# Performance work log

Hardware: AMD Instinct MI355X
Metric: run time of the kernel (lower is better)

Reference implementation:

```python
import jax, jax.numpy as jnp
import numpy as np

HID = 64        # HIDDEN_DIM
SLOTS = 6       # MEMORY_SLOTS
V = 64          # VOCAB_SIZE
NH = 2          # attention heads
THRESH = 0.5    # STAGE1_THRESH
EPS = 1e-5      # LayerNorm eps (torch default)


def setup_inputs() -> dict:
    key = jax.random.key(0)
    ks = jax.random.split(key, 16)
    B, L = 64, 1024
    def n(k, shape, s=0.05):
        return jax.random.normal(k, shape, jnp.float32) * s
    return {
        'seq':    jax.random.randint(ks[0], (B, L), 0, V),
        'query':  jax.random.randint(ks[1], (B,), 0, V),
        'target': jax.random.randint(ks[2], (B,), 0, V),
        # TinyEncoder params
        'embed':   n(ks[3], (V, HID)),
        'wqkv':    n(ks[4], (3 * HID, HID)), 'bqkv': jnp.zeros(3 * HID, jnp.float32),
        'wo_attn': n(ks[5], (HID, HID)),     'bo_attn': jnp.zeros(HID, jnp.float32),
        'w_ff1':   n(ks[6], (2 * HID, HID)), 'b_ff1': jnp.zeros(2 * HID, jnp.float32),
        'w_ff2':   n(ks[7], (HID, 2 * HID)), 'b_ff2': jnp.zeros(HID, jnp.float32),
        'g1': jnp.ones(HID, jnp.float32), 'be1': jnp.zeros(HID, jnp.float32),
        'g2': jnp.ones(HID, jnp.float32), 'be2': jnp.zeros(HID, jnp.float32),
        # gates
        'w_s1': n(ks[8], (1, HID)), 'b_s1': jnp.zeros(1, jnp.float32),
        'w_s2': n(ks[9], (1, HID)), 'b_s2': jnp.zeros(1, jnp.float32),
        # MemoryReader
        'w_qr': n(ks[10], (HID, HID)), 'b_qr': jnp.zeros(HID, jnp.float32),
        'w_or': n(ks[11], (V, HID)),   'b_or': jnp.zeros(V, jnp.float32),
        # query embedding
        'q_embed': n(ks[12], (V, HID)),
    }


def _layernorm(x, g, b):
    m = x.mean(-1, keepdims=True)
    v = ((x - m) ** 2).mean(-1, keepdims=True)
    return (x - m) * jax.lax.rsqrt(v + EPS) * g + b


def _mha(h, wqkv, bqkv, wo, bo):
    B, L, H = h.shape
    d = H // NH
    qkv = h @ wqkv.T + bqkv                      # [B,L,3H]
    q, k, v = jnp.split(qkv, 3, axis=-1)
    q = q.reshape(B, L, NH, d)
    k = k.reshape(B, L, NH, d)
    v = v.reshape(B, L, NH, d)
    scores = jnp.einsum('bqhd,bkhd->bhqk', q, k) / jnp.sqrt(jnp.float32(d))
    w = jax.nn.softmax(scores, axis=-1)          # [B,NH,L,L]
    o = jnp.einsum('bhqk,bkhd->bqhd', w, v).reshape(B, L, H)
    return o @ wo.T + bo


def reference(seq, query, target, embed, wqkv, bqkv, wo_attn, bo_attn,
              w_ff1, b_ff1, w_ff2, b_ff2, g1, be1, g2, be2,
              w_s1, b_s1, w_s2, b_s2, w_qr, b_qr, w_or, b_or, q_embed):
    # --- TinyEncoder ---
    h = embed[seq]                                           # [B,L,H]
    a = _mha(h, wqkv, bqkv, wo_attn, bo_attn)
    h = _layernorm(h + a, g1, be1)
    ff = jax.nn.relu(h @ w_ff1.T + b_ff1) @ w_ff2.T + b_ff2
    hidden = _layernorm(h + ff, g2, be2)                     # [B,L,H]

    # --- two-stage selection (vectorized; dead s1-branch elided) ---
    s1 = jax.nn.sigmoid(jnp.squeeze(hidden @ w_s1.T + b_s1, -1))   # [B,L]
    keep = (s1 > THRESH).astype(hidden.dtype)
    s2 = jax.nn.sigmoid(jnp.squeeze(hidden @ w_s2.T + b_s2, -1))
    s2f = s2 * keep
    _, topk = jax.lax.top_k(s2f, SLOTS)                            # [B,SLOTS]

    # --- gather memory slots ---
    mem = jnp.take_along_axis(hidden, topk[:, :, None], axis=1)    # [B,SLOTS,H]

    # --- MemoryReader ---
    q_h = q_embed[query]                                           # [B,H]
    q = q_h @ w_qr.T + b_qr                                        # [B,H]
    scores = (q[:, None, :] * mem).sum(-1) / jnp.sqrt(jnp.float32(HID))  # [B,SLOTS]
    w = jax.nn.softmax(scores, axis=-1)
    ctx = (w[:, :, None] * mem).sum(1)                             # [B,H]
    logits = ctx @ w_or.T + b_or                                   # [B,V]

    # --- cross entropy (mean) ---
    logp = jax.nn.log_softmax(logits, axis=-1)
    loss = -jnp.take_along_axis(logp, target[:, None], axis=1).mean()
    return loss
```

## Files before the change

kernel.cpp:

```cpp
#include <hip/hip_runtime.h>

#define DEV __device__ __forceinline__

DEV float wsum(float v){
  #pragma unroll
  for (int o = 32; o; o >>= 1) v += __shfl_xor(v, o, 64);
  return v;
}
DEV float wmax(float v){
  #pragma unroll
  for (int o = 32; o; o >>= 1) v = fmaxf(v, __shfl_xor(v, o, 64));
  return v;
}

__global__ __launch_bounds__(1024) void k_prep(
    const int* __restrict__ seq, const float* __restrict__ embed,
    const float* __restrict__ wqkv, const float* __restrict__ bqkv,
    float* __restrict__ qkv_tab, float* __restrict__ cnt_f,
    float* __restrict__ out){
  const int b = blockIdx.x, tid = threadIdx.x;
  if (b == 0 && tid == 0) out[0] = 0.f;
  __shared__ float emb[64];
  __shared__ int hh[64];
  if (tid < 64){ emb[tid] = embed[b*64 + tid]; hh[tid] = 0; }
  __syncthreads();
  atomicAdd(&hh[seq[b*1024 + tid]], 1);
  if (tid < 192){
    const float4* w4 = (const float4*)(wqkv + tid*64);
    float a0 = bqkv[tid], a1 = 0.f, a2 = 0.f, a3 = 0.f;
    #pragma unroll
    for (int k = 0; k < 16; k += 4){
      float4 wa = w4[k],   wb = w4[k+1], wc = w4[k+2], wd = w4[k+3];
      a0 += wa.x*emb[4*k]    + wa.y*emb[4*k+1]  + wa.z*emb[4*k+2]  + wa.w*emb[4*k+3];
      a1 += wb.x*emb[4*k+4]  + wb.y*emb[4*k+5]  + wb.z*emb[4*k+6]  + wb.w*emb[4*k+7];
      a2 += wc.x*emb[4*k+8]  + wc.y*emb[4*k+9]  + wc.z*emb[4*k+10] + wc.w*emb[4*k+11];
      a3 += wd.x*emb[4*k+12] + wd.y*emb[4*k+13] + wd.z*emb[4*k+14] + wd.w*emb[4*k+15];
    }
    qkv_tab[b*192 + tid] = (a0+a1)+(a2+a3);
  }
  __syncthreads();
  if (tid < 64) cnt_f[b*64 + tid] = (float)hh[tid];
}

__global__ __launch_bounds__(1024, 4) void k_enc(
    const float* __restrict__ qkv_tab, const float* __restrict__ cnt_f,
    const float* __restrict__ embed,
    const float* __restrict__ wo_attn, const float* __restrict__ bo_attn,
    const float* __restrict__ w_ff1, const float* __restrict__ b_ff1,
    const float* __restrict__ w_ff2, const float* __restrict__ b_ff2,
    const float* __restrict__ g1, const float* __restrict__ be1,
    const float* __restrict__ g2, const float* __restrict__ be2,
    const float* __restrict__ w_s1, const float* __restrict__ b_s1,
    const float* __restrict__ w_s2, const float* __restrict__ b_s2,
    float* __restrict__ hidden_tab, float* __restrict__ s2f_tab){
  const int b = blockIdx.x >> 2, quarter = blockIdx.x & 3;
  const int tid = threadIdx.x, wave = tid >> 6, lane = tid & 63;

  __shared__ float k_lds[64*65];
  __shared__ float v_lds[64*65];
  __shared__ float wo_lds[64*65];
  __shared__ float ff1_lds[128*65];
  __shared__ float ff2_lds[64*129];
  __shared__ float cnt_lds[64];
  __shared__ float xbuf[16][64];
  __shared__ float pbuf[16][128];

  for (int i = tid; i < 4096; i += 1024){
    int r = i >> 6, c = i & 63;
    k_lds[r*65 + c]  = qkv_tab[r*192 + 64 + c];
    v_lds[r*65 + c]  = qkv_tab[r*192 + 128 + c];
    wo_lds[r*65 + c] = wo_attn[i];
  }
  for (int i = tid; i < 8192; i += 1024){
    ff1_lds[(i >> 6)*65 + (i & 63)]   = w_ff1[i];
    ff2_lds[(i >> 7)*129 + (i & 127)] = w_ff2[i];
  }
  if (tid < 64) cnt_lds[tid] = cnt_f[b*64 + tid];
  __syncthreads();

  const float g1v = g1[lane],  be1v = be1[lane];
  const float g2v = g2[lane],  be2v = be2[lane];
  const float bov = bo_attn[lane], bf2v = b_ff2[lane];
  const float bf1a = b_ff1[lane], bf1b = b_ff1[64 + lane];
  const float ws1v = w_s1[lane], ws2v = w_s2[lane];
  const float bs1 = b_s1[0], bs2 = b_s2[0];
  const float cme = cnt_lds[lane];
  const bool  pres = cme > 0.f;
  const float sc = 0.17677669529663687f;
  const int   tok = quarter*16 + wave;

  const float qreg = qkv_tab[tok*192 + lane];
  xbuf[wave][lane] = qreg;
  __builtin_amdgcn_wave_barrier();
  float s0a = 0.f, s0b = 0.f, s1a = 0.f, s1b = 0.f;
  #pragma unroll
  for (int d = 0; d < 32; d += 2){
    s0a += xbuf[wave][d]      * k_lds[lane*65 + d];
    s0b += xbuf[wave][d+1]    * k_lds[lane*65 + d + 1];
    s1a += xbuf[wave][32+d]   * k_lds[lane*65 + 32 + d];
    s1b += xbuf[wave][32+d+1] * k_lds[lane*65 + 32 + d + 1];
  }
  float s0  = (s0a + s0b) * sc;
  float s1v = (s1a + s1b) * sc;
  float m0 = wmax(pres ? s0  : -1e30f);
  float m1 = wmax(pres ? s1v : -1e30f);
  float p0 = pres ? cme * __expf(s0  - m0) : 0.f;
  float p1 = pres ? cme * __expf(s1v - m1) : 0.f;
  float d0 = wsum(p0), d1 = wsum(p1);
  pbuf[wave][lane] = p0; pbuf[wave][64 + lane] = p1;
  __builtin_amdgcn_wave_barrier();
  const int pb = (lane & 32) << 1;
  float o0 = 0.f, o1 = 0.f, o2 = 0.f, o3 = 0.f;
  #pragma unroll
  for (int t = 0; t < 64; t += 4){
    o0 += pbuf[wave][pb + t]     * v_lds[t*65 + lane];
    o1 += pbuf[wave][pb + t + 1] * v_lds[(t+1)*65 + lane];
    o2 += pbuf[wave][pb + t + 2] * v_lds[(t+2)*65 + lane];
    o3 += pbuf[wave][pb + t + 3] * v_lds[(t+3)*65 + lane];
  }
  float o = ((o0 + o1) + (o2 + o3)) / (lane < 32 ? d0 : d1);
  xbuf[wave][lane] = o;
  __builtin_amdgcn_wave_barrier();
  float a0 = bov, a1 = 0.f, a2 = 0.f, a3 = 0.f;
  #pragma unroll
  for (int k = 0; k < 64; k += 4){
    a0 += wo_lds[lane*65 + k]     * xbuf[wave][k];
    a1 += wo_lds[lane*65 + k + 1] * xbuf[wave][k+1];
    a2 += wo_lds[lane*65 + k + 2] * xbuf[wave][k+2];
    a3 += wo_lds[lane*65 + k + 3] * xbuf[wave][k+3];
  }
  float a = (a0 + a1) + (a2 + a3);
  float x = embed[tok*64 + lane] + a;
  float mu = wsum(x) * 0.015625f;
  float xm = x - mu;
  float var = wsum(xm*xm) * 0.015625f;
  float xn = xm * rsqrtf(var + 1e-5f) * g1v + be1v;
  xbuf[wave][lane] = xn;
  __builtin_amdgcn_wave_barrier();
  float y0a = bf1a, y0b = 0.f, y1a = bf1b, y1b = 0.f;
  #pragma unroll
  for (int k = 0; k < 64; k += 2){
    float xk0 = xbuf[wave][k], xk1 = xbuf[wave][k+1];
    y0a += ff1_lds[lane*65 + k]          * xk0;
    y0b += ff1_lds[lane*65 + k + 1]      * xk1;
    y1a += ff1_lds[(lane+64)*65 + k]     * xk0;
    y1b += ff1_lds[(lane+64)*65 + k + 1] * xk1;
  }
  float y0 = fmaxf(y0a + y0b, 0.f), y1 = fmaxf(y1a + y1b, 0.f);
  pbuf[wave][lane] = y0; pbuf[wave][64 + lane] = y1;
  __builtin_amdgcn_wave_barrier();
  float z0 = bf2v, z1 = 0.f, z2 = 0.f, z3 = 0.f;
  #pragma unroll
  for (int j = 0; j < 128; j += 4){
    z0 += ff2_lds[lane*129 + j]     * pbuf[wave][j];
    z1 += ff2_lds[lane*129 + j + 1] * pbuf[wave][j+1];
    z2 += ff2_lds[lane*129 + j + 2] * pbuf[wave][j+2];
    z3 += ff2_lds[lane*129 + j + 3] * pbuf[wave][j+3];
  }
  float z = (z0 + z1) + (z2 + z3);
  float r = xn + z;
  float mu2 = wsum(r) * 0.015625f;
  float rm = r - mu2;
  float var2 = wsum(rm*rm) * 0.015625f;
  float hid = rm * rsqrtf(var2 + 1e-5f) * g2v + be2v;
  float t1 = wsum(hid * ws1v) + bs1;
  float t2 = wsum(hid * ws2v) + bs2;
  float sg1 = 1.f / (1.f + __expf(-t1));
  float sg2 = 1.f / (1.f + __expf(-t2));
  float s2f = (sg1 > 0.5f) ? sg2 : 0.f;

  hidden_tab[(b*64 + tok)*64 + lane] = hid;
  if (lane == 0) s2f_tab[b*64 + tok] = s2f;
}

__global__ __launch_bounds__(64) void k_sel(
    const int* __restrict__ seq, const int* __restrict__ query,
    const int* __restrict__ target,
    const float* __restrict__ hidden_tab, const float* __restrict__ s2f_tab,
    const float* __restrict__ w_qr, const float* __restrict__ b_qr,
    const float* __restrict__ w_or, const float* __restrict__ b_or,
    const float* __restrict__ q_embed, float* __restrict__ out){
  const int b = blockIdx.x, lane = threadIdx.x;
  __shared__ float s2_lds[64];
  __shared__ float wq_lds[64*65];
  __shared__ float wor_lds[64*65];
  s2_lds[lane] = s2f_tab[b*64 + lane];
  #pragma unroll 8
  for (int j = 0; j < 64; ++j){
    wq_lds[j*65 + lane]  = w_qr[j*64 + lane];
    wor_lds[j*65 + lane] = w_or[j*64 + lane];
  }
  __builtin_amdgcn_wave_barrier();

  float vals[16];
  #pragma unroll
  for (int j = 0; j < 16; ++j){
    int tk = seq[b*1024 + j*64 + lane];
    vals[j] = s2_lds[tk];
  }
  int sel[6];
  #pragma unroll
  for (int r = 0; r < 6; ++r){
    float bv = -1.f; int bi = 1 << 30;
    #pragma unroll
    for (int j = 0; j < 16; ++j){
      float v = vals[j]; int i = (j << 6) | lane;
      if (v > bv || (v == bv && i < bi)){ bv = v; bi = i; }
    }
    #pragma unroll
    for (int o = 32; o; o >>= 1){
      float ov = __shfl_xor(bv, o, 64);
      int   oi = __shfl_xor(bi, o, 64);
      if (ov > bv || (ov == bv && oi < bi)){ bv = ov; bi = oi; }
    }
    sel[r] = bi;
    int jw = bi >> 6, lw = bi & 63;
    if (lane == lw){
      #pragma unroll
      for (int j = 0; j < 16; ++j) if (j == jw) vals[j] = -1.f;
    }
  }

  float mem[6];
  #pragma unroll
  for (int s = 0; s < 6; ++s){
    int tk = seq[b*1024 + sel[s]];
    mem[s] = hidden_tab[(b*64 + tk)*64 + lane];
  }
  float qe = q_embed[query[b]*64 + lane];
  float qv0 = b_qr[lane], qv1 = 0.f, qv2 = 0.f, qv3 = 0.f;
  #pragma unroll
  for (int k = 0; k < 64; k += 4){
    qv0 += wq_lds[lane*65 + k]     * __shfl(qe, k, 64);
    qv1 += wq_lds[lane*65 + k + 1] * __shfl(qe, k+1, 64);
    qv2 += wq_lds[lane*65 + k + 2] * __shfl(qe, k+2, 64);
    qv3 += wq_lds[lane*65 + k + 3] * __shfl(qe, k+3, 64);
  }
  float qv = (qv0 + qv1) + (qv2 + qv3);
  float scv[6];
  #pragma unroll
  for (int s = 0; s < 6; ++s) scv[s] = wsum(qv * mem[s]) * 0.125f;
  float mx = scv[0];
  #pragma unroll
  for (int s = 1; s < 6; ++s) mx = fmaxf(mx, scv[s]);
  float e[6], se = 0.f;
  #pragma unroll
  for (int s = 0; s < 6; ++s){ e[s] = __expf(scv[s] - mx); se += e[s]; }
  float ctx = 0.f;
  #pragma unroll
  for (int s = 0; s < 6; ++s) ctx += (e[s] / se) * mem[s];
  float l0 = b_or[lane], l1 = 0.f, l2 = 0.f, l3 = 0.f;
  #pragma unroll
  for (int k = 0; k < 64; k += 4){
    l0 += wor_lds[lane*65 + k]     * __shfl(ctx, k, 64);
    l1 += wor_lds[lane*65 + k + 1] * __shfl(ctx, k+1, 64);
    l2 += wor_lds[lane*65 + k + 2] * __shfl(ctx, k+2, 64);
    l3 += wor_lds[lane*65 + k + 3] * __shfl(ctx, k+3, 64);
  }
  float lg = (l0 + l1) + (l2 + l3);
  float lm = wmax(lg);
  float ss = wsum(__expf(lg - lm));
  float lt = __shfl(lg, target[b], 64);
  if (lane == 0) atomicAdd(out, -(lt - lm - __logf(ss)) * 0.015625f);
}

extern "C" void kernel_launch(void* const* d_in, const int* in_sizes, int n_in,
                              void* d_out, int out_size, void* d_ws, size_t ws_size,
                              hipStream_t stream){
  const int*   seq     = (const int*)  d_in[0];
  const int*   query   = (const int*)  d_in[1];
  const int*   target  = (const int*)  d_in[2];
  const float* embed   = (const float*)d_in[3];
  const float* wqkv    = (const float*)d_in[4];
  const float* bqkv    = (const float*)d_in[5];
  const float* wo_attn = (const float*)d_in[6];
  const float* bo_attn = (const float*)d_in[7];
  const float* w_ff1   = (const float*)d_in[8];
  const float* b_ff1   = (const float*)d_in[9];
  const float* w_ff2   = (const float*)d_in[10];
  const float* b_ff2   = (const float*)d_in[11];
  const float* g1      = (const float*)d_in[12];
  const float* be1     = (const float*)d_in[13];
  const float* g2      = (const float*)d_in[14];
  const float* be2     = (const float*)d_in[15];
  const float* w_s1    = (const float*)d_in[16];
  const float* b_s1    = (const float*)d_in[17];
  const float* w_s2    = (const float*)d_in[18];
  const float* b_s2    = (const float*)d_in[19];
  const float* w_qr    = (const float*)d_in[20];
  const float* b_qr    = (const float*)d_in[21];
  const float* w_or    = (const float*)d_in[22];
  const float* b_or    = (const float*)d_in[23];
  const float* q_embed = (const float*)d_in[24];

  float* ws = (float*)d_ws;
  float* qkv_tab    = ws;
  float* cnt_f      = ws + 12288;
  float* hidden_tab = ws + 16384;
  float* s2f_tab    = ws + 278528;

  float* out = (float*)d_out;

  k_prep<<<64, 1024, 0, stream>>>(seq, embed, wqkv, bqkv, qkv_tab, cnt_f, out);
  k_enc<<<256, 1024, 0, stream>>>(qkv_tab, cnt_f, embed, wo_attn, bo_attn,
                                  w_ff1, b_ff1, w_ff2, b_ff2, g1, be1, g2, be2,
                                  w_s1, b_s1, w_s2, b_s2, hidden_tab, s2f_tab);
  k_sel<<<64, 64, 0, stream>>>(seq, query, target, hidden_tab, s2f_tab,
                               w_qr, b_qr, w_or, b_or, q_embed, out);
}
```

Before: 136.9 us.

## Process four tokens per wave in encoder with swizzled float4 LDS and readlane broadcasts

Result: no change. 135.2 us (-1.2%).

```diff
diff --git a/kernel.cpp b/kernel.cpp
--- a/kernel.cpp
+++ b/kernel.cpp
@@ -1,6 +1,27 @@
 #include <hip/hip_runtime.h>
 
 #define DEV __device__ __forceinline__
+
+DEV int   f2i(float v){ return __builtin_bit_cast(int, v); }
+DEV float i2f(int v){ return __builtin_bit_cast(float, v); }
+DEV float blane(float v, int l){ return i2f(__builtin_amdgcn_readlane(f2i(v), l)); }
+
+template<int C> DEV float dpp_add(float v){
+  return v + i2f(__builtin_amdgcn_update_dpp(0, f2i(v), C, 0xF, 0xF, true));
+}
+template<int C> DEV float dpp_max(float v){
+  return fmaxf(v, i2f(__builtin_amdgcn_update_dpp(0, f2i(v), C, 0xF, 0xF, true)));
+}
+DEV float wred_sum(float v){
+  v = dpp_add<0xB1>(v); v = dpp_add<0x4E>(v); v = dpp_add<0x141>(v); v = dpp_add<0x140>(v);
+  v += i2f(__builtin_amdgcn_ds_swizzle(f2i(v), 0x401F));
+  return blane(v, 0) + blane(v, 32);
+}
+DEV float wred_max(float v){
+  v = dpp_max<0xB1>(v); v = dpp_max<0x4E>(v); v = dpp_max<0x141>(v); v = dpp_max<0x140>(v);
+  v = fmaxf(v, i2f(__builtin_amdgcn_ds_swizzle(f2i(v), 0x401F)));
+  return fmaxf(blane(v, 0), blane(v, 32));
+}
 
 DEV float wsum(float v){
   #pragma unroll
@@ -42,7 +63,7 @@
   if (tid < 64) cnt_f[b*64 + tid] = (float)hh[tid];
 }
 
-__global__ __launch_bounds__(1024, 4) void k_enc(
+__global__ __launch_bounds__(256, 2) void k_enc(
     const float* __restrict__ qkv_tab, const float* __restrict__ cnt_f,
     const float* __restrict__ embed,
     const float* __restrict__ wo_attn, const float* __restrict__ bo_attn,
@@ -54,123 +75,173 @@
     const float* __restrict__ w_s2, const float* __restrict__ b_s2,
     float* __restrict__ hidden_tab, float* __restrict__ s2f_tab){
   const int b = blockIdx.x >> 2, quarter = blockIdx.x & 3;
-  const int tid = threadIdx.x, wave = tid >> 6, lane = tid & 63;
-
-  __shared__ float k_lds[64*65];
-  __shared__ float v_lds[64*65];
-  __shared__ float wo_lds[64*65];
-  __shared__ float ff1_lds[128*65];
-  __shared__ float ff2_lds[64*129];
-  __shared__ float cnt_lds[64];
-  __shared__ float xbuf[16][64];
-  __shared__ float pbuf[16][128];
-
-  for (int i = tid; i < 4096; i += 1024){
-    int r = i >> 6, c = i & 63;
-    k_lds[r*65 + c]  = qkv_tab[r*192 + 64 + c];
-    v_lds[r*65 + c]  = qkv_tab[r*192 + 128 + c];
-    wo_lds[r*65 + c] = wo_attn[i];
-  }
-  for (int i = tid; i < 8192; i += 1024){
-    ff1_lds[(i >> 6)*65 + (i & 63)]   = w_ff1[i];
-    ff2_lds[(i >> 7)*129 + (i & 127)] = w_ff2[i];
+  const int tid = threadIdx.x, w = tid >> 6, lane = tid & 63;
+
+  __shared__ float4 k4 [64*16];
+  __shared__ float4 v4t[64*16];
+  __shared__ float4 wo4[64*16];
+  __shared__ float4 f14[128*16];
+  __shared__ float4 f24[64*32];
+  __shared__ float4 pb4[4][64][2];
+  __shared__ float  cnt_lds[64];
+
+  const float4* qkv4 = (const float4*)qkv_tab;
+  const float4* wo_4 = (const float4*)wo_attn;
+  const float4* f1_4 = (const float4*)w_ff1;
+  const float4* f2_4 = (const float4*)w_ff2;
+  float* v4f = (float*)v4t;
+
+  #pragma unroll
+  for (int ii = 0; ii < 4; ++ii){
+    int i = tid + ii*256;
+    int r = i >> 4, c4 = i & 15, s = c4 ^ (r & 15);
+    k4 [r*16 + s] = qkv4[r*48 + 16 + c4];
+    wo4[r*16 + s] = wo_4[i];
+    float4 vv = qkv4[r*48 + 32 + c4];
+    int d0 = 4*c4;
+    v4f[(d0  )*64 + 4*((r>>2) ^ ((d0  )&15)) + (r&3)] = vv.x;
+    v4f[(d0+1)*64 + 4*((r>>2) ^ ((d0+1)&15)) + (r&3)] = vv.y;
+    v4f[(d0+2)*64 + 4*((r>>2) ^ ((d0+2)&15)) + (r&3)] = vv.z;
+    v4f[(d0+3)*64 + 4*((r>>2) ^ ((d0+3)&15)) + (r&3)] = vv.w;
+  }
+  #pragma unroll
+  for (int ii = 0; ii < 8; ++ii){
+    int i = tid + ii*256;
+    int r1 = i >> 4, c41 = i & 15;
+    f14[r1*16 + (c41 ^ (r1 & 15))] = f1_4[i];
+    int r2 = i >> 5, c42 = i & 31;
+    f24[r2*32 + (c42 ^ (r2 & 15))] = f2_4[i];
   }
   if (tid < 64) cnt_lds[tid] = cnt_f[b*64 + tid];
   __syncthreads();
 
-  const float g1v = g1[lane],  be1v = be1[lane];
-  const float g2v = g2[lane],  be2v = be2[lane];
-  const float bov = bo_attn[lane], bf2v = b_ff2[lane];
-  const float bf1a = b_ff1[lane], bf1b = b_ff1[64 + lane];
-  const float ws1v = w_s1[lane], ws2v = w_s2[lane];
-  const float bs1 = b_s1[0], bs2 = b_s2[0];
-  const float cme = cnt_lds[lane];
+  const int   t0 = quarter*16 + w*4;
+  const int   sw = lane & 15;
+  const int   h2 = lane >> 5;
+  const float cme  = cnt_lds[lane];
   const bool  pres = cme > 0.f;
   const float sc = 0.17677669529663687f;
-  const int   tok = quarter*16 + wave;
-
-  const float qreg = qkv_tab[tok*192 + lane];
-  xbuf[wave][lane] = qreg;
+  const float g1v=g1[lane], be1v=be1[lane], g2v=g2[lane], be2v=be2[lane];
+  const float bov=bo_attn[lane], bf2v=b_ff2[lane];
+  const float bf1a=b_ff1[lane], bf1b=b_ff1[64+lane];
+  const float ws1v=w_s1[lane], ws2v=w_s2[lane];
+  const float bs1=b_s1[0], bs2=b_s2[0];
+
+  float q0 = qkv_tab[(t0+0)*192 + lane];
+  float q1 = qkv_tab[(t0+1)*192 + lane];
+  float q2 = qkv_tab[(t0+2)*192 + lane];
+  float q3 = qkv_tab[(t0+3)*192 + lane];
+  float sA[4] = {0.f,0.f,0.f,0.f}, sB[4] = {0.f,0.f,0.f,0.f};
+  #pragma unroll
+  for (int c4 = 0; c4 < 16; ++c4){
+    float4 kk = k4[lane*16 + (c4 ^ sw)];
+    #pragma unroll
+    for (int j = 0; j < 4; ++j){
+      const int d = 4*c4 + j;
+      float ke = (j==0)?kk.x:(j==1)?kk.y:(j==2)?kk.z:kk.w;
+      float b0 = blane(q0,d), b1 = blane(q1,d), b2 = blane(q2,d), b3 = blane(q3,d);
+      if (d < 32){ sA[0]+=b0*ke; sA[1]+=b1*ke; sA[2]+=b2*ke; sA[3]+=b3*ke; }
+      else       { sB[0]+=b0*ke; sB[1]+=b1*ke; sB[2]+=b2*ke; sB[3]+=b3*ke; }
+    }
+  }
+  float p0[4], p1[4], d0v[4], d1v[4];
+  #pragma unroll
+  for (int t = 0; t < 4; ++t){
+    float s0 = sA[t]*sc, s1 = sB[t]*sc;
+    float m0 = wred_max(pres ? s0 : -1e30f);
+    float m1 = wred_max(pres ? s1 : -1e30f);
+    p0[t] = pres ? cme*__expf(s0 - m0) : 0.f;
+    p1[t] = pres ? cme*__expf(s1 - m1) : 0.f;
+    d0v[t] = wred_sum(p0[t]);
+    d1v[t] = wred_sum(p1[t]);
+  }
+  pb4[w][lane][0] = make_float4(p0[0],p0[1],p0[2],p0[3]);
+  pb4[w][lane][1] = make_float4(p1[0],p1[1],p1[2],p1[3]);
   __builtin_amdgcn_wave_barrier();
-  float s0a = 0.f, s0b = 0.f, s1a = 0.f, s1b = 0.f;
-  #pragma unroll
-  for (int d = 0; d < 32; d += 2){
-    s0a += xbuf[wave][d]      * k_lds[lane*65 + d];
-    s0b += xbuf[wave][d+1]    * k_lds[lane*65 + d + 1];
-    s1a += xbuf[wave][32+d]   * k_lds[lane*65 + 32 + d];
-    s1b += xbuf[wave][32+d+1] * k_lds[lane*65 + 32 + d + 1];
-  }
-  float s0  = (s0a + s0b) * sc;
-  float s1v = (s1a + s1b) * sc;
-  float m0 = wmax(pres ? s0  : -1e30f);
-  float m1 = wmax(pres ? s1v : -1e30f);
-  float p0 = pres ? cme * __expf(s0  - m0) : 0.f;
-  float p1 = pres ? cme * __expf(s1v - m1) : 0.f;
-  float d0 = wsum(p0), d1 = wsum(p1);
-  pbuf[wave][lane] = p0; pbuf[wave][64 + lane] = p1;
-  __builtin_amdgcn_wave_barrier();
-  const int pb = (lane & 32) << 1;
-  float o0 = 0.f, o1 = 0.f, o2 = 0.f, o3 = 0.f;
-  #pragma unroll
-  for (int t = 0; t < 64; t += 4){
-    o0 += pbuf[wave][pb + t]     * v_lds[t*65 + lane];
-    o1 += pbuf[wave][pb + t + 1] * v_lds[(t+1)*65 + lane];
-    o2 += pbuf[wave][pb + t + 2] * v_lds[(t+2)*65 + lane];
-    o3 += pbuf[wave][pb + t + 3] * v_lds[(t+3)*65 + lane];
-  }
-  float o = ((o0 + o1) + (o2 + o3)) / (lane < 32 ? d0 : d1);
-  xbuf[wave][lane] = o;
-  __builtin_amdgcn_wave_barrier();
-  float a0 = bov, a1 = 0.f, a2 = 0.f, a3 = 0.f;
-  #pragma unroll
-  for (int k = 0; k < 64; k += 4){
-    a0 += wo_lds[lane*65 + k]     * xbuf[wave][k];
-    a1 += wo_lds[lane*65 + k + 1] * xbuf[wave][k+1];
-    a2 += wo_lds[lane*65 + k + 2] * xbuf[wave][k+2];
-    a3 += wo_lds[lane*65 + k + 3] * xbuf[wave][k+3];
-  }
-  float a = (a0 + a1) + (a2 + a3);
-  float x = embed[tok*64 + lane] + a;
-  float mu = wsum(x) * 0.015625f;
-  float xm = x - mu;
-  float var = wsum(xm*xm) * 0.015625f;
-  float xn = xm * rsqrtf(var + 1e-5f) * g1v + be1v;
-  xbuf[wave][lane] = xn;
-  __builtin_amdgcn_wave_barrier();
-  float y0a = bf1a, y0b = 0.f, y1a = bf1b, y1b = 0.f;
-  #pragma unroll
-  for (int k = 0; k < 64; k += 2){
-    float xk0 = xbuf[wave][k], xk1 = xbuf[wave][k+1];
-    y0a += ff1_lds[lane*65 + k]          * xk0;
-    y0b += ff1_lds[lane*65 + k + 1]      * xk1;
-    y1a += ff1_lds[(lane+64)*65 + k]     * xk0;
-    y1b += ff1_lds[(lane+64)*65 + k + 1] * xk1;
-  }
-  float y0 = fmaxf(y0a + y0b, 0.f), y1 = fmaxf(y1a + y1b, 0.f);
-  pbuf[wave][lane] = y0; pbuf[wave][64 + lane] = y1;
-  __builtin_amdgcn_wave_barrier();
-  float z0 = bf2v, z1 = 0.f, z2 = 0.f, z3 = 0.f;
-  #pragma unroll
-  for (int j = 0; j < 128; j += 4){
-    z0 += ff2_lds[lane*129 + j]     * pbuf[wave][j];
-    z1 += ff2_lds[lane*129 + j + 1] * pbuf[wave][j+1];
-    z2 += ff2_lds[lane*129 + j + 2] * pbuf[wave][j+2];
-    z3 += ff2_lds[lane*129 + j + 3] * pbuf[wave][j+3];
-  }
-  float z = (z0 + z1) + (z2 + z3);
-  float r = xn + z;
-  float mu2 = wsum(r) * 0.015625f;
-  float rm = r - mu2;
-  float var2 = wsum(rm*rm) * 0.015625f;
-  float hid = rm * rsqrtf(var2 + 1e-5f) * g2v + be2v;
-  float t1 = wsum(hid * ws1v) + bs1;
-  float t2 = wsum(hid * ws2v) + bs2;
-  float sg1 = 1.f / (1.f + __expf(-t1));
-  float sg2 = 1.f / (1.f + __expf(-t2));
-  float s2f = (sg1 > 0.5f) ? sg2 : 0.f;
-
-  hidden_tab[(b*64 + tok)*64 + lane] = hid;
-  if (lane == 0) s2f_tab[b*64 + tok] = s2f;
+  float o[4] = {0.f,0.f,0.f,0.f};
+  #pragma unroll
+  for (int c4 = 0; c4 < 16; ++c4){
+    float4 vv = v4t[lane*16 + (c4 ^ sw)];
+    #pragma unroll
+    for (int j = 0; j < 4; ++j){
+      const int tp = 4*c4 + j;
+      float ve = (j==0)?vv.x:(j==1)?vv.y:(j==2)?vv.z:vv.w;
+      float4 pp = pb4[w][tp][h2];
+      o[0] += pp.x*ve; o[1] += pp.y*ve; o[2] += pp.z*ve; o[3] += pp.w*ve;
+    }
+  }
+  #pragma unroll
+  for (int t = 0; t < 4; ++t) o[t] /= (lane < 32 ? d0v[t] : d1v[t]);
+  float aT[4] = {bov,bov,bov,bov};
+  #pragma unroll
+  for (int c4 = 0; c4 < 16; ++c4){
+    float4 ww = wo4[lane*16 + (c4 ^ sw)];
+    #pragma unroll
+    for (int j = 0; j < 4; ++j){
+      const int k = 4*c4 + j;
+      float we = (j==0)?ww.x:(j==1)?ww.y:(j==2)?ww.z:ww.w;
+      aT[0] += we*blane(o[0],k); aT[1] += we*blane(o[1],k);
+      aT[2] += we*blane(o[2],k); aT[3] += we*blane(o[3],k);
+    }
+  }
+  float xn[4];
+  #pragma unroll
+  for (int t = 0; t < 4; ++t){
+    float x = embed[(t0+t)*64 + lane] + aT[t];
+    float mu = wred_sum(x) * 0.015625f;
+    float xm = x - mu;
+    float var = wred_sum(xm*xm) * 0.015625f;
+    xn[t] = xm * rsqrtf(var + 1e-5f) * g1v + be1v;
+  }
+  float y0[4] = {bf1a,bf1a,bf1a,bf1a}, y1[4] = {bf1b,bf1b,bf1b,bf1b};
+  #pragma unroll
+  for (int c4 = 0; c4 < 16; ++c4){
+    float4 wA = f14[lane*16 + (c4 ^ sw)];
+    float4 wB = f14[(lane+64)*16 + (c4 ^ sw)];
+    #pragma unroll
+    for (int j = 0; j < 4; ++j){
+      const int k = 4*c4 + j;
+      float wa = (j==0)?wA.x:(j==1)?wA.y:(j==2)?wA.z:wA.w;
+      float wb = (j==0)?wB.x:(j==1)?wB.y:(j==2)?wB.z:wB.w;
+      float x0 = blane(xn[0],k), x1 = blane(xn[1],k), x2 = blane(xn[2],k), x3 = blane(xn[3],k);
+      y0[0]+=wa*x0; y0[1]+=wa*x1; y0[2]+=wa*x2; y0[3]+=wa*x3;
+      y1[0]+=wb*x0; y1[1]+=wb*x1; y1[2]+=wb*x2; y1[3]+=wb*x3;
+    }
+  }
+  #pragma unroll
+  for (int t = 0; t < 4; ++t){ y0[t] = fmaxf(y0[t],0.f); y1[t] = fmaxf(y1[t],0.f); }
+  float z[4] = {bf2v,bf2v,bf2v,bf2v};
+  #pragma unroll
+  for (int c4 = 0; c4 < 32; ++c4){
+    float4 ww = f24[lane*32 + (c4 ^ sw)];
+    #pragma unroll
+    for (int j = 0; j < 4; ++j){
+      const int jj = 4*c4 + j;
+      float we = (j==0)?ww.x:(j==1)?ww.y:(j==2)?ww.z:ww.w;
+      if (jj < 64){
+        z[0]+=we*blane(y0[0],jj); z[1]+=we*blane(y0[1],jj);
+        z[2]+=we*blane(y0[2],jj); z[3]+=we*blane(y0[3],jj);
+      } else {
+        z[0]+=we*blane(y1[0],jj-64); z[1]+=we*blane(y1[1],jj-64);
+        z[2]+=we*blane(y1[2],jj-64); z[3]+=we*blane(y1[3],jj-64);
+      }
+    }
+  }
+  #pragma unroll
+  for (int t = 0; t < 4; ++t){
+    float r = xn[t] + z[t];
+    float mu2 = wred_sum(r) * 0.015625f;
+    float rm = r - mu2;
+    float var2 = wred_sum(rm*rm) * 0.015625f;
+    float hid = rm * rsqrtf(var2 + 1e-5f) * g2v + be2v;
+    float t1 = wred_sum(hid * ws1v) + bs1;
+    float t2 = wred_sum(hid * ws2v) + bs2;
+    float sg1 = 1.f / (1.f + __expf(-t1));
+    float sg2 = 1.f / (1.f + __expf(-t2));
+    float s2f = (sg1 > 0.5f) ? sg2 : 0.f;
+    hidden_tab[(b*64 + t0 + t)*64 + lane] = hid;
+    if (lane == 0) s2f_tab[b*64 + t0 + t] = s2f;
+  }
 }
 
 __global__ __launch_bounds__(64) void k_sel(
@@ -302,9 +373,9 @@
   float* out = (float*)d_out;
 
   k_prep<<<64, 1024, 0, stream>>>(seq, embed, wqkv, bqkv, qkv_tab, cnt_f, out);
-  k_enc<<<256, 1024, 0, stream>>>(qkv_tab, cnt_f, embed, wo_attn, bo_attn,
-                                  w_ff1, b_ff1, w_ff2, b_ff2, g1, be1, g2, be2,
-                                  w_s1, b_s1, w_s2, b_s2, hidden_tab, s2f_tab);
+  k_enc<<<256, 256, 0, stream>>>(qkv_tab, cnt_f, embed, wo_attn, bo_attn,
+                                 w_ff1, b_ff1, w_ff2, b_ff2, g1, be1, g2, be2,
+                                 w_s1, b_s1, w_s2, b_s2, hidden_tab, s2f_tab);
   k_sel<<<64, 64, 0, stream>>>(seq, query, target, hidden_tab, s2f_tab,
                                w_qr, b_qr, w_or, b_or, q_embed, out);
 }
```
